# Kernel tuning notes

Measured on AMD Instinct MI355X. Metric: run time of the kernel, lower is better.

Reference implementation:

```python
import jax, jax.numpy as jnp
import numpy as np

T = 5          # temporal frames
WS = 8         # window size (square)
HEADS = 6
DIM = 192      # output channels; qkv input channels = 3*DIM
SHIFT = WS // 2
HDIM = DIM // HEADS
SCALE = HDIM ** -0.5
N = T * WS * WS  # tokens per window = 320


def _rel_index():
    # Faithful replication of the torch buffer construction (including the
    # quirk that the dw channel gets no offset).
    coords = np.stack(np.meshgrid(np.arange(T), np.arange(WS), np.arange(WS), indexing='ij'))
    cf = coords.reshape(3, -1)                      # (3, N)
    rel = (cf[:, :, None] - cf[:, None, :]).transpose(1, 2, 0).astype(np.int64)
    rel[:, :, 0] += WS - 1                          # dt channel
    rel[:, :, 1] += WS - 1                          # dh channel
    rel[:, :, 0] *= 2 * WS - 1
    return rel.sum(-1)                               # (N, N) int

REL_INDEX = jnp.asarray(_rel_index())


def setup_inputs() -> dict:
    key = jax.random.key(0)
    k1, k2, k3, k4 = jax.random.split(key, 4)
    B, H, W = 2, 64, 64
    C = 3 * DIM
    qkv = jax.random.normal(k1, (B, T * H * W, C), jnp.float32)
    bias_table = jax.random.normal(k2, ((T * 2 * WS - 1) * (2 * WS - 1), HEADS), jnp.float32) * 0.02
    proj_w = jax.random.normal(k3, (DIM, DIM), jnp.float32) / np.sqrt(DIM)
    proj_b = jax.random.normal(k4, (DIM,), jnp.float32) * 0.01
    # Standard Swin shifted-window attention mask, tiled over T (t-outer order).
    img = np.zeros((H, W), np.float32)
    cnt = 0
    sls = (slice(0, -WS), slice(-WS, -SHIFT), slice(-SHIFT, None))
    for hs in sls:
        for ws_ in sls:
            img[hs, ws_] = cnt
            cnt += 1
    mw = img.reshape(H // WS, WS, W // WS, WS).transpose(0, 2, 1, 3).reshape(-1, WS * WS)
    mw = np.tile(mw, (1, T))                         # (nW, N)
    am = mw[:, None, :] - mw[:, :, None]
    mask = jnp.asarray(np.where(am != 0, -100.0, 0.0).astype(np.float32))
    return {'qkv': qkv, 'bias_table': bias_table, 'proj_w': proj_w,
            'proj_b': proj_b, 'mask': mask, 'H': H, 'W': W}


def reference(qkv, bias_table, proj_w, proj_b, mask, H, W):
    B, L, C = qkv.shape
    x = qkv.reshape(B, T, H, W, C)
    # cyclic shift
    x = jnp.roll(x, shift=(-SHIFT, -SHIFT), axis=(2, 3))
    # window partition -> (B*nW, N, C)
    x = x.reshape(B, T, H // WS, WS, W // WS, WS, C)
    x = x.transpose(0, 2, 4, 1, 3, 5, 6).reshape(-1, N, C)
    B_ = x.shape[0]
    qkv_ = x.reshape(B_, N, 3, HEADS, HDIM).transpose(2, 0, 3, 1, 4)  # (3,B_,h,N,d)
    q, k, v = qkv_[0] * SCALE, qkv_[1], qkv_[2]
    attn = jnp.einsum('bhqd,bhkd->bhqk', q, k)       # (B_, h, N, N)
    rpb = bias_table[REL_INDEX.reshape(-1)].reshape(N, N, HEADS).transpose(2, 0, 1)
    attn = attn + rpb[None]
    nW = mask.shape[0]
    attn = attn.reshape(B_ // nW, nW, HEADS, N, N) + mask[None, :, None]
    attn = jax.nn.softmax(attn.reshape(B_, HEADS, N, N), axis=-1)
    out = jnp.einsum('bhqk,bhkd->bhqd', attn, v)     # (B_, h, N, d)
    out = out.transpose(0, 2, 1, 3).reshape(B_, N, DIM)
    out = out @ proj_w.T + proj_b
    # window reverse -> (B, T, H, W, DIM)
    out = out.reshape(B, H // WS, W // WS, T, WS, WS, DIM)
    out = out.transpose(0, 3, 1, 4, 2, 5, 6).reshape(B, T, H, W, DIM)
    out = jnp.roll(out, shift=(SHIFT, SHIFT), axis=(2, 3))
    return out.reshape(B, T * H * W, DIM)
```

## Files before the change

kernel.cpp:

```cpp
#include <hip/hip_runtime.h>
#include <hip/hip_bf16.h>

#define TT      5
#define NHEADS  6
#define DIMC    192
#define SHIFT_  4
#define HDIM_   32
#define NTOK    320
#define NWIN    64
#define BATCH   2
#define LOG2E   1.44269504088896f
#define SCALE_LOG2E (0.17677669529663687f * 1.44269504088896f)
#define NEGMASK (-100.0f * 1.44269504088896f)

typedef short short8v __attribute__((ext_vector_type(8)));
typedef float floatx4 __attribute__((ext_vector_type(4)));
union FragU { uint4 u; short8v s; };

static __device__ __forceinline__ float bf16lo(unsigned u) {
    union { unsigned i; float f; } x; x.i = u << 16; return x.f;
}
static __device__ __forceinline__ float bf16hi(unsigned u) {
    union { unsigned i; float f; } x; x.i = u & 0xffff0000u; return x.f;
}
static __device__ __forceinline__ unsigned short bf16b(float f) {
    __hip_bfloat16 h = __float2bfloat16(f);
    unsigned short u; __builtin_memcpy(&u, &h, 2); return u;
}
static __device__ __forceinline__ unsigned pk2(float a, float b) {
    return (unsigned)bf16b(a) | ((unsigned)bf16b(b) << 16);
}
static __device__ __forceinline__ unsigned pk2h(float a, float b) {
    unsigned ua = __float_as_uint(a), ub = __float_as_uint(b);
    return ((ua + 0x8000u) >> 16) | ((ub + 0x8000u) & 0xffff0000u);
}

static __device__ __forceinline__ bool detect_bf16(const unsigned* q) {
    uint4 w = ((const uint4*)q)[threadIdx.x & 63];
    int cnt = 0;
    unsigned e;
    e = (w.x >> 7) & 0xffu; cnt += (e >= 100u && e <= 135u);
    e = (w.y >> 7) & 0xffu; cnt += (e >= 100u && e <= 135u);
    e = (w.z >> 7) & 0xffu; cnt += (e >= 100u && e <= 135u);
    e = (w.w >> 7) & 0xffu; cnt += (e >= 100u && e <= 135u);
    unsigned long long m = __ballot(cnt >= 2);
    return __popcll(m) >= 32;
}

__global__ __launch_bounds__(NTOK) void attn_mfma(
    const void* __restrict__ qkv_raw,
    const void* __restrict__ bias_raw,
    __hip_bfloat16* __restrict__ win_out)
{
    const bool isbf = detect_bf16((const unsigned*)qkv_raw);
    const int b_  = blockIdx.x;
    const int h   = blockIdx.y;
    const int bb  = b_ >> 6;
    const int wdx = b_ & 63;
    const int wi  = wdx >> 3, wj = wdx & 7;
    const int tid = threadIdx.x;
    const int w    = tid >> 6;
    const int lane = tid & 63;
    const int l15  = lane & 15;
    const int quad = lane >> 4;
    const int g    = lane >> 3;
    const int li   = lane & 7;

    __shared__ unsigned short sK[320 * 40];
    __shared__ unsigned short sVT[32 * 328];
    __shared__ float sBias[192];

    if (tid < 192)
        sBias[tid] = (isbf ? __bfloat162float(((const __hip_bfloat16*)bias_raw)[tid * NHEADS + h])
                           : ((const float*)bias_raw)[tid * NHEADS + h]) * LOG2E;

    {
        const int btok = w * 64;
        if (!isbf) {
            const float* q32 = (const float*)qkv_raw;
            #pragma unroll
            for (int r = 0; r < 8; r++) {
                const int token = btok + r * 8 + g;
                const int t = token >> 6, s = token & 63;
                const int gh = (wi * 8 + (s >> 3) + SHIFT_) & 63;
                const int gw = (wj * 8 + (s & 7) + SHIFT_) & 63;
                const long grow = (long)bb * (TT * 64 * 64) + t * 4096 + gh * 64 + gw;
                const float4 kv = *(const float4*)(q32 + grow * (3 * DIMC) + DIMC + h * HDIM_ + li * 4);
                const int l32 = token & 31;
                const int slot = (token & ~31) + ((l32 & 4) << 2) + ((l32 >> 3) << 2) + (l32 & 3);
                *(uint2*)&sK[slot * 40 + li * 4] = make_uint2(pk2(kv.x, kv.y), pk2(kv.z, kv.w));
            }
            #pragma unroll
            for (int r = 0; r < 8; r++) {
                const int token = btok + r * 8 + g;
                const int t = token >> 6, s = token & 63;
                const int gh = (wi * 8 + (s >> 3) + SHIFT_) & 63;
                const int gw = (wj * 8 + (s & 7) + SHIFT_) & 63;
                const long grow = (long)bb * (TT * 64 * 64) + t * 4096 + gh * 64 + gw;
                const float4 vv = *(const float4*)(q32 + grow * (3 * DIMC) + 2 * DIMC + h * HDIM_ + li * 4);
                const int d0 = li * 4;
                sVT[(d0 + 0) * 328 + token] = bf16b(vv.x);
                sVT[(d0 + 1) * 328 + token] = bf16b(vv.y);
                sVT[(d0 + 2) * 328 + token] = bf16b(vv.z);
                sVT[(d0 + 3) * 328 + token] = bf16b(vv.w);
            }
        } else {
            const unsigned short* q16 = (const unsigned short*)qkv_raw;
            #pragma unroll
            for (int r = 0; r < 8; r++) {
                const int token = btok + r * 8 + g;
                const int t = token >> 6, s = token & 63;
                const int gh = (wi * 8 + (s >> 3) + SHIFT_) & 63;
                const int gw = (wj * 8 + (s & 7) + SHIFT_) & 63;
                const long grow = (long)bb * (TT * 64 * 64) + t * 4096 + gh * 64 + gw;
                const uint2 kv = *(const uint2*)(q16 + grow * (3 * DIMC) + DIMC + h * HDIM_ + li * 4);
                const int l32 = token & 31;
                const int slot = (token & ~31) + ((l32 & 4) << 2) + ((l32 >> 3) << 2) + (l32 & 3);
                *(uint2*)&sK[slot * 40 + li * 4] = kv;
            }
            #pragma unroll
            for (int r = 0; r < 8; r++) {
                const int token = btok + r * 8 + g;
                const int t = token >> 6, s = token & 63;
                const int gh = (wi * 8 + (s >> 3) + SHIFT_) & 63;
                const int gw = (wj * 8 + (s & 7) + SHIFT_) & 63;
                const long grow = (long)bb * (TT * 64 * 64) + t * 4096 + gh * 64 + gw;
                const uint2 vv = *(const uint2*)(q16 + grow * (3 * DIMC) + 2 * DIMC + h * HDIM_ + li * 4);
                const int d0 = li * 4;
                sVT[(d0 + 0) * 328 + token] = (unsigned short)(vv.x & 0xffffu);
                sVT[(d0 + 1) * 328 + token] = (unsigned short)(vv.x >> 16);
                sVT[(d0 + 2) * 328 + token] = (unsigned short)(vv.y & 0xffffu);
                sVT[(d0 + 3) * 328 + token] = (unsigned short)(vv.y >> 16);
            }
        }
    }

    FragU qf[4];
    int cn_q[4], labq[4];
    #pragma unroll
    for (int jq = 0; jq < 4; jq++) {
        const int qtok = w * 64 + jq * 16 + l15;
        const int t = qtok >> 6, s = qtok & 63, hl = s >> 3, wl = s & 7;
        cn_q[jq] = t * 15 + hl + wl;
        const int hh = wi * 8 + hl, ww = wj * 8 + wl;
        labq[jq] = ((hh < 56) ? 0 : ((hh < 60) ? 1 : 2)) * 3 +
                   ((ww < 56) ? 0 : ((ww < 60) ? 1 : 2));
        const int gh = (wi * 8 + hl + SHIFT_) & 63;
        const int gw = (wj * 8 + wl + SHIFT_) & 63;
        const long grow = (long)bb * (TT * 64 * 64) + t * 4096 + gh * 64 + gw;
        if (!isbf) {
            const float* qp = (const float*)qkv_raw + grow * (3 * DIMC) + h * HDIM_ + quad * 8;
            qf[jq].u = make_uint4(
                pk2(qp[0]*SCALE_LOG2E, qp[1]*SCALE_LOG2E), pk2(qp[2]*SCALE_LOG2E, qp[3]*SCALE_LOG2E),
                pk2(qp[4]*SCALE_LOG2E, qp[5]*SCALE_LOG2E), pk2(qp[6]*SCALE_LOG2E, qp[7]*SCALE_LOG2E));
        } else {
            const uint4 uu = *(const uint4*)((const __hip_bfloat16*)qkv_raw + grow * (3 * DIMC) + h * HDIM_ + quad * 8);
            qf[jq].u = make_uint4(
                pk2(bf16lo(uu.x)*SCALE_LOG2E, bf16hi(uu.x)*SCALE_LOG2E),
                pk2(bf16lo(uu.y)*SCALE_LOG2E, bf16hi(uu.y)*SCALE_LOG2E),
                pk2(bf16lo(uu.z)*SCALE_LOG2E, bf16hi(uu.z)*SCALE_LOG2E),
                pk2(bf16lo(uu.w)*SCALE_LOG2E, bf16hi(uu.w)*SCALE_LOG2E));
        }
    }
    __syncthreads();

    const floatx4 z4 = {0.f, 0.f, 0.f, 0.f};
    floatx4 oacc[4][2];
    #pragma unroll
    for (int i = 0; i < 4; i++) { oacc[i][0] = z4; oacc[i][1] = z4; }
    float rs[4] = {0.f, 0.f, 0.f, 0.f};

    for (int kb = 0; kb < 10; kb++) {
        FragU kf0, kf1, vf0, vf1;
        kf0.u = *(const uint4*)&sK[(kb * 32 + l15) * 40 + quad * 8];
        kf1.u = *(const uint4*)&sK[(kb * 32 + 16 + l15) * 40 + quad * 8];
        vf0.u = *(const uint4*)&sVT[l15 * 328 + kb * 32 + quad * 8];
        vf1.u = *(const uint4*)&sVT[(16 + l15) * 328 + kb * 32 + quad * 8];

        floatx4 sv0[4], sv1[4];
        #pragma unroll
        for (int jq = 0; jq < 4; jq++)
            sv0[jq] = __builtin_amdgcn_mfma_f32_16x16x32_bf16(kf0.s, qf[jq].s, z4, 0, 0, 0);
        #pragma unroll
        for (int jq = 0; jq < 4; jq++)
            sv1[jq] = __builtin_amdgcn_mfma_f32_16x16x32_bf16(kf1.s, qf[jq].s, z4, 0, 0, 0);

        const int Ck   = (7 - (kb >> 1)) * 15 + 7;
        const int sh   = (kb & 1) * 4 + quad;
        const int rhk  = (wi == 7) ? ((sh < 4) ? 1 : 2) : 0;
        const int lab0 = rhk * 3 + ((wj == 7) ? 1 : 0);
        const int lab1 = rhk * 3 + ((wj == 7) ? 2 : 0);
        const int cb   = Ck - sh;

        #pragma unroll
        for (int jq = 0; jq < 4; jq++) {
            const int bidx = cn_q[jq] + cb;
            const float m0 = (lab0 != labq[jq]) ? NEGMASK : 0.f;
            const float m1 = (lab1 != labq[jq]) ? NEGMASK : 0.f;
            float e0[4], e1[4];
            #pragma unroll
            for (int reg = 0; reg < 4; reg++)
                e0[reg] = exp2f(sv0[jq][reg] + sBias[bidx - reg] + m0);
            #pragma unroll
            for (int reg = 0; reg < 4; reg++)
                e1[reg] = exp2f(sv1[jq][reg] + sBias[bidx - 4 - reg] + m1);
            rs[jq] += ((e0[0] + e0[1]) + (e0[2] + e0[3]))
                    + ((e1[0] + e1[1]) + (e1[2] + e1[3]));
            FragU pf;
            pf.u.x = pk2h(e0[0], e0[1]); pf.u.y = pk2h(e0[2], e0[3]);
            pf.u.z = pk2h(e1[0], e1[1]); pf.u.w = pk2h(e1[2], e1[3]);
            oacc[jq][0] = __builtin_amdgcn_mfma_f32_16x16x32_bf16(vf0.s, pf.s, oacc[jq][0], 0, 0, 0);
            oacc[jq][1] = __builtin_amdgcn_mfma_f32_16x16x32_bf16(vf1.s, pf.s, oacc[jq][1], 0, 0, 0);
        }
    }

    unsigned short* wp = (unsigned short*)win_out;
    #pragma unroll
    for (int jq = 0; jq < 4; jq++) {
        float r = rs[jq];
        r += __shfl_xor(r, 16);
        r += __shfl_xor(r, 32);
        const float inv = 1.0f / r;
        const long ob = ((long)b_ * NTOK + (w * 64 + jq * 16 + l15)) * DIMC + h * HDIM_ + quad * 4;
        #pragma unroll
        for (int nt = 0; nt < 2; nt++) {
            const floatx4 o = oacc[jq][nt];
            *(uint2*)&wp[ob + nt * 16] =
                make_uint2(pk2(o[0] * inv, o[1] * inv), pk2(o[2] * inv, o[3] * inv));
        }
    }
}

__global__ __launch_bounds__(256) void prep_w(
    const void* __restrict__ w_raw, const void* __restrict__ b_raw,
    const unsigned* __restrict__ sniff,
    unsigned short* __restrict__ wbf, float* __restrict__ bf32)
{
    const bool isbf = detect_bf16(sniff);
    const int g = blockIdx.x * 256 + threadIdx.x;
    if (!isbf) wbf[g] = bf16b(((const float*)w_raw)[g]);
    else       wbf[g] = ((const unsigned short*)w_raw)[g];
    if (blockIdx.x == 0 && threadIdx.x < 192) {
        bf32[threadIdx.x] = isbf
            ? __bfloat162float(((const __hip_bfloat16*)b_raw)[threadIdx.x])
            : ((const float*)b_raw)[threadIdx.x];
    }
}

__global__ __launch_bounds__(256) void proj_mfma(
    const __hip_bfloat16* __restrict__ win,
    const unsigned short* __restrict__ wbf,
    const float* __restrict__ bf32,
    const unsigned* __restrict__ sniff,
    void* __restrict__ out_raw)
{
    const bool isbf = detect_bf16(sniff);
    const int tid  = threadIdx.x;
    const int w    = tid >> 6;
    const int lane = tid & 63;
    const int l15  = lane & 15;
    const int quad = lane >> 4;
    const int tok0 = blockIdx.x * 64 + w * 16;

    const floatx4 z4 = {0.f, 0.f, 0.f, 0.f};
    floatx4 acc[12];
    #pragma unroll
    for (int nt = 0; nt < 12; nt++) acc[nt] = z4;

    #pragma unroll
    for (int ks = 0; ks < 6; ks++) {
        FragU xf;
        xf.u = *(const uint4*)((const unsigned short*)win + ((long)tok0 + l15) * DIMC + ks * 32 + quad * 8);
        #pragma unroll
        for (int nt = 0; nt < 12; nt++) {
            FragU wf;
            wf.u = *(const uint4*)(wbf + (nt * 16 + l15) * DIMC + ks * 32 + quad * 8);
            acc[nt] = __builtin_amdgcn_mfma_f32_16x16x32_bf16(wf.s, xf.s, acc[nt], 0, 0, 0);
        }
    }

    const int token = tok0 + l15;
    const int bw = token / NTOK;
    const int nn = token - bw * NTOK;
    const int bb = bw >> 6, wdx = bw & 63, wi2 = wdx >> 3, wj2 = wdx & 7;
    const int t = nn >> 6, s2 = nn & 63, hl = s2 >> 3, wl = s2 & 7;
    const int gh = (wi2 * 8 + hl + SHIFT_) & 63;
    const int gw = (wj2 * 8 + wl + SHIFT_) & 63;
    const long rowoff = ((long)bb * (TT * 64 * 64) + t * 4096 + gh * 64 + gw) * DIMC;

    #pragma unroll
    for (int nt = 0; nt < 12; nt++) {
        const float4 bv = *(const float4*)&bf32[nt * 16 + quad * 4];
        const float o0 = acc[nt][0] + bv.x, o1 = acc[nt][1] + bv.y;
        const float o2 = acc[nt][2] + bv.z, o3 = acc[nt][3] + bv.w;
        const long off = rowoff + nt * 16 + quad * 4;
        if (!isbf) {
            *(float4*)((float*)out_raw + off) = make_float4(o0, o1, o2, o3);
        } else {
            *(uint2*)((unsigned short*)out_raw + off) = make_uint2(pk2(o0, o1), pk2(o2, o3));
        }
    }
}

extern "C" void kernel_launch(void* const* d_in, const int* in_sizes, int n_in,
                              void* d_out, int out_size, void* d_ws, size_t ws_size,
                              hipStream_t stream)
{
    (void)in_sizes; (void)n_in; (void)out_size; (void)ws_size;
    const void* qkv        = d_in[0];
    const void* bias_table = d_in[1];
    const void* proj_w     = d_in[2];
    const void* proj_b     = d_in[3];

    __hip_bfloat16* win = (__hip_bfloat16*)d_ws;
    unsigned short* wbf = (unsigned short*)((char*)d_ws + 15728640);
    float*          bfb = (float*)((char*)d_ws + 15802368);

    prep_w<<<dim3(144), 256, 0, stream>>>(proj_w, proj_b, (const unsigned*)qkv, wbf, bfb);
    attn_mfma<<<dim3(BATCH * NWIN, NHEADS), NTOK, 0, stream>>>(qkv, bias_table, win);
    proj_mfma<<<dim3(BATCH * NWIN * NTOK / 64), 256, 0, stream>>>(
        win, wbf, bfb, (const unsigned*)qkv, d_out);
}
```

Measured before the change: 249.0 us.

## Precompute full relative position bias per head and use raw v_exp_f32

Adds a prep kernel that expands the relative position bias table into a dense per-head (6x320x320) fp32 matrix, pre-scaled by log2e, stored in workspace. The attention kernel reads the bias from global memory as float4 vectors instead of gathering from a small LDS table. It also replaces exp2f with inline v_exp_f32 asm. This removes the LDS gathers and the index arithmetic, but adds about 2.4MB of global bias reads per head-window pass, served mostly from cache, plus extra work in the prep kernel.

```diff
diff --git a/kernel.cpp b/kernel.cpp
--- a/kernel.cpp
+++ b/kernel.cpp
@@ -34,6 +34,11 @@
     unsigned ua = __float_as_uint(a), ub = __float_as_uint(b);
     return ((ua + 0x8000u) >> 16) | ((ub + 0x8000u) & 0xffff0000u);
 }
+static __device__ __forceinline__ float fexp2(float x) {
+    float r;
+    asm("v_exp_f32 %0, %1" : "=v"(r) : "v"(x));
+    return r;
+}
 
 static __device__ __forceinline__ bool detect_bf16(const unsigned* q) {
     uint4 w = ((const uint4*)q)[threadIdx.x & 63];
@@ -49,7 +54,7 @@
 
 __global__ __launch_bounds__(NTOK) void attn_mfma(
     const void* __restrict__ qkv_raw,
-    const void* __restrict__ bias_raw,
+    const float* __restrict__ rpb,
     __hip_bfloat16* __restrict__ win_out)
 {
     const bool isbf = detect_bf16((const unsigned*)qkv_raw);
@@ -68,11 +73,6 @@
 
     __shared__ unsigned short sK[320 * 40];
     __shared__ unsigned short sVT[32 * 328];
-    __shared__ float sBias[192];
-
-    if (tid < 192)
-        sBias[tid] = (isbf ? __bfloat162float(((const __hip_bfloat16*)bias_raw)[tid * NHEADS + h])
-                           : ((const float*)bias_raw)[tid * NHEADS + h]) * LOG2E;
 
     {
         const int btok = w * 64;
@@ -136,12 +136,13 @@
     }
 
     FragU qf[4];
-    int cn_q[4], labq[4];
+    int labq[4];
+    const float* rq[4];
     #pragma unroll
     for (int jq = 0; jq < 4; jq++) {
         const int qtok = w * 64 + jq * 16 + l15;
         const int t = qtok >> 6, s = qtok & 63, hl = s >> 3, wl = s & 7;
-        cn_q[jq] = t * 15 + hl + wl;
+        rq[jq] = rpb + ((h * NTOK + qtok) * NTOK);
         const int hh = wi * 8 + hl, ww = wj * 8 + wl;
         labq[jq] = ((hh < 56) ? 0 : ((hh < 60) ? 1 : 2)) * 3 +
                    ((ww < 56) ? 0 : ((ww < 60) ? 1 : 2));
@@ -177,6 +178,14 @@
         vf0.u = *(const uint4*)&sVT[l15 * 328 + kb * 32 + quad * 8];
         vf1.u = *(const uint4*)&sVT[(16 + l15) * 328 + kb * 32 + quad * 8];
 
+        float4 rb0[4], rb1[4];
+        #pragma unroll
+        for (int jq = 0; jq < 4; jq++) {
+            const float* rp = rq[jq] + kb * 32 + quad * 8;
+            rb0[jq] = *(const float4*)rp;
+            rb1[jq] = *(const float4*)(rp + 4);
+        }
+
         floatx4 sv0[4], sv1[4];
         #pragma unroll
         for (int jq = 0; jq < 4; jq++)
@@ -185,25 +194,24 @@
         for (int jq = 0; jq < 4; jq++)
             sv1[jq] = __builtin_amdgcn_mfma_f32_16x16x32_bf16(kf1.s, qf[jq].s, z4, 0, 0, 0);
 
-        const int Ck   = (7 - (kb >> 1)) * 15 + 7;
         const int sh   = (kb & 1) * 4 + quad;
         const int rhk  = (wi == 7) ? ((sh < 4) ? 1 : 2) : 0;
         const int lab0 = rhk * 3 + ((wj == 7) ? 1 : 0);
         const int lab1 = rhk * 3 + ((wj == 7) ? 2 : 0);
-        const int cb   = Ck - sh;
 
         #pragma unroll
         for (int jq = 0; jq < 4; jq++) {
-            const int bidx = cn_q[jq] + cb;
             const float m0 = (lab0 != labq[jq]) ? NEGMASK : 0.f;
             const float m1 = (lab1 != labq[jq]) ? NEGMASK : 0.f;
             float e0[4], e1[4];
-            #pragma unroll
-            for (int reg = 0; reg < 4; reg++)
-                e0[reg] = exp2f(sv0[jq][reg] + sBias[bidx - reg] + m0);
-            #pragma unroll
-            for (int reg = 0; reg < 4; reg++)
-                e1[reg] = exp2f(sv1[jq][reg] + sBias[bidx - 4 - reg] + m1);
+            e0[0] = fexp2(sv0[jq][0] + rb0[jq].x + m0);
+            e0[1] = fexp2(sv0[jq][1] + rb0[jq].y + m0);
+            e0[2] = fexp2(sv0[jq][2] + rb0[jq].z + m0);
+            e0[3] = fexp2(sv0[jq][3] + rb0[jq].w + m0);
+            e1[0] = fexp2(sv1[jq][0] + rb1[jq].x + m1);
+            e1[1] = fexp2(sv1[jq][1] + rb1[jq].y + m1);
+            e1[2] = fexp2(sv1[jq][2] + rb1[jq].z + m1);
+            e1[3] = fexp2(sv1[jq][3] + rb1[jq].w + m1);
             rs[jq] += ((e0[0] + e0[1]) + (e0[2] + e0[3]))
                     + ((e1[0] + e1[1]) + (e1[2] + e1[3]));
             FragU pf;
@@ -231,19 +239,35 @@
     }
 }
 
-__global__ __launch_bounds__(256) void prep_w(
+__global__ __launch_bounds__(256) void prep_all(
     const void* __restrict__ w_raw, const void* __restrict__ b_raw,
+    const void* __restrict__ bias_raw,
     const unsigned* __restrict__ sniff,
-    unsigned short* __restrict__ wbf, float* __restrict__ bf32)
+    unsigned short* __restrict__ wbf, float* __restrict__ bf32,
+    float* __restrict__ rpb)
 {
     const bool isbf = detect_bf16(sniff);
-    const int g = blockIdx.x * 256 + threadIdx.x;
-    if (!isbf) wbf[g] = bf16b(((const float*)w_raw)[g]);
-    else       wbf[g] = ((const unsigned short*)w_raw)[g];
-    if (blockIdx.x == 0 && threadIdx.x < 192) {
-        bf32[threadIdx.x] = isbf
-            ? __bfloat162float(((const __hip_bfloat16*)b_raw)[threadIdx.x])
-            : ((const float*)b_raw)[threadIdx.x];
+    const int gid = blockIdx.x * 256 + threadIdx.x;
+    if (gid < 36864) {
+        if (!isbf) wbf[gid] = bf16b(((const float*)w_raw)[gid]);
+        else       wbf[gid] = ((const unsigned short*)w_raw)[gid];
+    }
+    if (gid < 192) {
+        bf32[gid] = isbf
+            ? __bfloat162float(((const __hip_bfloat16*)b_raw)[gid])
+            : ((const float*)b_raw)[gid];
+    }
+    const int q = gid / NTOK;
+    const int k = gid - q * NTOK;
+    const int cnq = (q >> 6) * 15 + ((q >> 3) & 7) + (q & 7);
+    const int cnk = (k >> 6) * 15 + ((k >> 3) & 7) + (k & 7);
+    const int idx = (cnq - cnk + 112) * NHEADS;
+    #pragma unroll
+    for (int h = 0; h < NHEADS; h++) {
+        const float v = isbf
+            ? __bfloat162float(((const __hip_bfloat16*)bias_raw)[idx + h])
+            : ((const float*)bias_raw)[idx + h];
+        rpb[(h * NTOK + q) * NTOK + k] = v * LOG2E;
     }
 }
 
@@ -315,9 +339,11 @@
     __hip_bfloat16* win = (__hip_bfloat16*)d_ws;
     unsigned short* wbf = (unsigned short*)((char*)d_ws + 15728640);
     float*          bfb = (float*)((char*)d_ws + 15802368);
-
-    prep_w<<<dim3(144), 256, 0, stream>>>(proj_w, proj_b, (const unsigned*)qkv, wbf, bfb);
-    attn_mfma<<<dim3(BATCH * NWIN, NHEADS), NTOK, 0, stream>>>(qkv, bias_table, win);
+    float*          rpb = (float*)((char*)d_ws + 15803136);
+
+    prep_all<<<dim3(400), 256, 0, stream>>>(proj_w, proj_b, bias_table,
+                                            (const unsigned*)qkv, wbf, bfb, rpb);
+    attn_mfma<<<dim3(BATCH * NWIN, NHEADS), NTOK, 0, stream>>>(qkv, rpb, win);
     proj_mfma<<<dim3(BATCH * NWIN * NTOK / 64), 256, 0, stream>>>(
         win, wbf, bfb, (const unsigned*)qkv, d_out);
 }
```

New measurement: 250.5 us. Within noise of the previous version (+0.6%).
